# Optimization experiments

Measured on AMD Instinct MI355X. Metric: run time of the kernel, lower is better.

The kernel has to match this reference:

```python
import jax, jax.numpy as jnp
import numpy as np

N, D, E = 100000, 128, 600000  # nodes, feature dim, edges
EPS = 1e-5  # BatchNorm1d default eps


def setup_inputs() -> dict:
    key = jax.random.key(0)
    k = jax.random.split(key, 4)
    x = jax.random.normal(k[0], (N, D), jnp.float32)
    edge_index = jax.random.randint(k[1], (2, E), 0, N, jnp.int32)  # [src; dst]
    W = jax.random.normal(k[2], (D, D), jnp.float32) * (1.0 / np.sqrt(D))
    b = jnp.zeros((D,), jnp.float32)
    gamma = jnp.ones((D,), jnp.float32)
    beta = jnp.zeros((D,), jnp.float32)
    return dict(x=x, edge_index=edge_index, W=W, b=b, gamma=gamma, beta=beta)


def reference(x, edge_index, W, b, gamma, beta):
    # dropout p=0 -> identity
    src, dst = edge_index[0], edge_index[1]
    ones = jnp.ones((E,), x.dtype)
    deg_out = jnp.maximum(jax.ops.segment_sum(ones, src, num_segments=N), 1.0)
    deg_in = jnp.maximum(jax.ops.segment_sum(ones, dst, num_segments=N), 1.0)
    # GraphConv norm='both': D_out^{-1/2} on src side, sum-aggregate, D_in^{-1/2} on dst side
    h = x * jax.lax.rsqrt(deg_out)[:, None]            # [N, D]
    agg = jax.ops.segment_sum(h[src], dst, num_segments=N)  # gather+scatter over edges
    agg = agg * jax.lax.rsqrt(deg_in)[:, None]
    new_x = agg @ W + b                                 # linear after aggregation
    # residual (num_dst_nodes == N for a homogeneous graph)
    h = x + new_x
    # BatchNorm1d, training-mode batch statistics (biased variance)
    mean = jnp.mean(h, axis=0)
    var = jnp.var(h, axis=0)
    h = (h - mean) * jax.lax.rsqrt(var + EPS) * gamma + beta
    return jax.nn.relu(h)
```

## Files before the change

kernel.cpp:

```cpp
#include <hip/hip_runtime.h>
#include <math.h>

#define D 128
#define NGB 512
#define SLOTS 32
constexpr float EPS = 1e-5f;

typedef short v8s __attribute__((ext_vector_type(8)));
typedef float v4f __attribute__((ext_vector_type(4)));

__device__ __forceinline__ unsigned short f2bf(float f) {
    union { float f; unsigned u; } c; c.f = f;
    unsigned u = c.u;
    return (unsigned short)((u + 0x7FFFu + ((u >> 16) & 1u)) >> 16);
}
__device__ __forceinline__ float bf2f(unsigned short u) {
    union { unsigned u; float f; } c; c.u = ((unsigned)u) << 16; return c.f;
}

__global__ void fused_bucket_kernel(const int* __restrict__ src, const int* __restrict__ dst,
                                    int* __restrict__ deg_in, int* __restrict__ deg_out8,
                                    int* __restrict__ esrc, int n, int E) {
    int e = blockIdx.x * blockDim.x + threadIdx.x;
    if (e >= E) return;
    int s = src[e], d = dst[e];
    int pos = atomicAdd(&deg_in[d], 1);
    if (pos < SLOTS) esrc[((size_t)d << 5) | pos] = s;
    atomicAdd(&deg_out8[(size_t)(blockIdx.x & 7) * n + s], 1);
}

__global__ void rsdeg_kernel(const int* __restrict__ deg_out8, float* __restrict__ rs_out, int n) {
    int v = blockIdx.x * blockDim.x + threadIdx.x;
    if (v < n) {
        int s = 0;
        #pragma unroll
        for (int p = 0; p < 8; ++p) s += deg_out8[(size_t)p * n + v];
        rs_out[v] = rsqrtf(fmaxf((float)s, 1.0f));
    }
}

__global__ void xscale_kernel(const float4* __restrict__ x4, const float* __restrict__ rs_out,
                              ushort4* __restrict__ xb4, int total4) {
    int stride = gridDim.x * blockDim.x;
    for (int f = blockIdx.x * blockDim.x + threadIdx.x; f < total4; f += stride) {
        int row = f >> 5;
        float sc = rs_out[row];
        float4 v = x4[f];
        ushort4 o;
        o.x = f2bf(v.x * sc); o.y = f2bf(v.y * sc);
        o.z = f2bf(v.z * sc); o.w = f2bf(v.w * sc);
        xb4[f] = o;
    }
}

__global__ __launch_bounds__(256)
void agg_kernel(const ushort4* __restrict__ xb4, const int* __restrict__ deg_in,
                const int* __restrict__ esrc, ushort4* __restrict__ aggb4, int n) {
    int g = blockIdx.x * 8 + (threadIdx.x >> 5);
    int l32 = threadIdx.x & 31;
    if (g >= n) return;
    int deg = deg_in[g];
    int cnt = min(deg, SLOTS);
    const int* base = esrc + ((size_t)g << 5);
    float4 acc = make_float4(0.f, 0.f, 0.f, 0.f);
    int e = 0;
    for (; e + 3 < cnt; e += 4) {
        int s0 = base[e], s1 = base[e + 1], s2 = base[e + 2], s3 = base[e + 3];
        ushort4 u0 = xb4[(size_t)s0 * 32 + l32];
        ushort4 u1 = xb4[(size_t)s1 * 32 + l32];
        ushort4 u2 = xb4[(size_t)s2 * 32 + l32];
        ushort4 u3 = xb4[(size_t)s3 * 32 + l32];
        acc.x += bf2f(u0.x) + bf2f(u1.x) + bf2f(u2.x) + bf2f(u3.x);
        acc.y += bf2f(u0.y) + bf2f(u1.y) + bf2f(u2.y) + bf2f(u3.y);
        acc.z += bf2f(u0.z) + bf2f(u1.z) + bf2f(u2.z) + bf2f(u3.z);
        acc.w += bf2f(u0.w) + bf2f(u1.w) + bf2f(u2.w) + bf2f(u3.w);
    }
    for (; e < cnt; ++e) {
        int s0 = base[e];
        ushort4 u0 = xb4[(size_t)s0 * 32 + l32];
        acc.x += bf2f(u0.x);
        acc.y += bf2f(u0.y);
        acc.z += bf2f(u0.z);
        acc.w += bf2f(u0.w);
    }
    float si = rsqrtf(fmaxf((float)deg, 1.0f));
    ushort4 o;
    o.x = f2bf(acc.x * si);
    o.y = f2bf(acc.y * si);
    o.z = f2bf(acc.z * si);
    o.w = f2bf(acc.w * si);
    aggb4[(size_t)g * 32 + l32] = o;
}

__global__ void wconv_kernel(const float* __restrict__ W, ushort* __restrict__ wfrag) {
    int t = blockIdx.x * 256 + threadIdx.x;
    int lane = t & 63;
    int nt = (t >> 6) & 7;
    int kt = t >> 9;
    int n = nt * 16 + (lane & 15);
    int k0 = kt * 32 + (lane >> 4) * 8;
    ushort* dst = wfrag + (size_t)t * 8;
    #pragma unroll
    for (int j = 0; j < 8; ++j) dst[j] = f2bf(W[(size_t)(k0 + j) * D + n]);
}

__global__ __launch_bounds__(256, 2)
void gemm_mfma_kernel(const v8s* __restrict__ aggb8,
                      const v8s* __restrict__ wfrag8,
                      const float* __restrict__ b,
                      const float* __restrict__ x,
                      float* __restrict__ out,
                      float* __restrict__ bnpart, int n) {
    const int lane = threadIdx.x & 63;
    const int wave = threadIdx.x >> 6;
    const int gwave = blockIdx.x * 4 + wave;
    const int nwaves = gridDim.x * 4;
    const int ntiles = (n + 15) >> 4;
    const int c = lane & 15;
    const int s = lane >> 4;

    v8s wf[4][8];
    #pragma unroll
    for (int kt = 0; kt < 4; ++kt)
        #pragma unroll
        for (int nt = 0; nt < 8; ++nt)
            wf[kt][nt] = wfrag8[(kt * 8 + nt) * 64 + lane];

    float bv[8];
    #pragma unroll
    for (int nt = 0; nt < 8; ++nt) bv[nt] = b[nt * 16 + c];

    float hs[8], hq[8];
    #pragma unroll
    for (int nt = 0; nt < 8; ++nt) { hs[nt] = 0.f; hq[nt] = 0.f; }

    for (int tile = gwave; tile < ntiles; tile += nwaves) {
        const int row0 = tile * 16;
        int arow = row0 + c;
        if (arow >= n) arow = n - 1;

        v4f acc[8];
        #pragma unroll
        for (int nt = 0; nt < 8; ++nt) acc[nt] = (v4f)(0.f);

        #pragma unroll
        for (int kt = 0; kt < 4; ++kt) {
            v8s af = aggb8[(size_t)arow * 16 + kt * 4 + s];
            #pragma unroll
            for (int nt = 0; nt < 8; ++nt)
                acc[nt] = __builtin_amdgcn_mfma_f32_16x16x32_bf16(af, wf[kt][nt], acc[nt], 0, 0, 0);
        }

        #pragma unroll
        for (int j = 0; j < 4; ++j) {
            int m = row0 + s * 4 + j;
            if (m < n) {
                const float* xr = x + (size_t)m * D;
                float* orow = out + (size_t)m * D;
                #pragma unroll
                for (int nt = 0; nt < 8; ++nt) {
                    float h = acc[nt][j] + bv[nt] + xr[nt * 16 + c];
                    orow[nt * 16 + c] = h;
                    hs[nt] += h;
                    hq[nt] += h * h;
                }
            }
        }
    }

    #pragma unroll
    for (int nt = 0; nt < 8; ++nt) {
        hs[nt] += __shfl_xor(hs[nt], 16); hs[nt] += __shfl_xor(hs[nt], 32);
        hq[nt] += __shfl_xor(hq[nt], 16); hq[nt] += __shfl_xor(hq[nt], 32);
    }
    __shared__ float ls[4][128];
    __shared__ float lq[4][128];
    if (s == 0) {
        #pragma unroll
        for (int nt = 0; nt < 8; ++nt) {
            ls[wave][nt * 16 + c] = hs[nt];
            lq[wave][nt * 16 + c] = hq[nt];
        }
    }
    __syncthreads();
    const int t = threadIdx.x;
    if (t < 128) {
        float a = ls[0][t] + ls[1][t] + ls[2][t] + ls[3][t];
        bnpart[(size_t)t * NGB + blockIdx.x] = a;
    } else {
        int cc = t - 128;
        float a = lq[0][cc] + lq[1][cc] + lq[2][cc] + lq[3][cc];
        bnpart[(size_t)(128 + cc) * NGB + blockIdx.x] = a;
    }
}

__global__ __launch_bounds__(256)
void stats2_kernel(const float* __restrict__ partial, float* __restrict__ stats) {
    const int idx = blockIdx.x;
    const int t = threadIdx.x;
    float a = partial[(size_t)idx * NGB + t] + partial[(size_t)idx * NGB + 256 + t];
    #pragma unroll
    for (int off = 32; off >= 1; off >>= 1) a += __shfl_xor(a, off);
    __shared__ float w[4];
    if ((t & 63) == 0) w[t >> 6] = a;
    __syncthreads();
    if (t == 0) stats[idx] = w[0] + w[1] + w[2] + w[3];
}

__global__ void params_kernel(const float* __restrict__ stats, const float* __restrict__ gamma,
                              const float* __restrict__ beta, float* __restrict__ scale,
                              float* __restrict__ shift, float inv_n) {
    int c = threadIdx.x;
    if (c < D) {
        float mean = stats[c] * inv_n;
        float var = fmaxf(stats[D + c] * inv_n - mean * mean, 0.f);
        float inv = rsqrtf(var + EPS);
        float sc = gamma[c] * inv;
        scale[c] = sc;
        shift[c] = beta[c] - mean * sc;
    }
}

__global__ void final_kernel(float4* __restrict__ h4, const float4* __restrict__ scale4,
                             const float4* __restrict__ shift4, int total4) {
    int stride = gridDim.x * blockDim.x;
    for (int f = blockIdx.x * blockDim.x + threadIdx.x; f < total4; f += stride) {
        int c4 = f & 31;
        float4 v = h4[f];
        float4 s = scale4[c4];
        float4 sh = shift4[c4];
        float4 r;
        r.x = fmaxf(fmaf(v.x, s.x, sh.x), 0.f);
        r.y = fmaxf(fmaf(v.y, s.y, sh.y), 0.f);
        r.z = fmaxf(fmaf(v.z, s.z, sh.z), 0.f);
        r.w = fmaxf(fmaf(v.w, s.w, sh.w), 0.f);
        h4[f] = r;
    }
}

extern "C" void kernel_launch(void* const* d_in, const int* in_sizes, int n_in,
                              void* d_out, int out_size, void* d_ws, size_t ws_size,
                              hipStream_t stream) {
    const float* x     = (const float*)d_in[0];
    const int*   ei    = (const int*)d_in[1];
    const float* W     = (const float*)d_in[2];
    const float* b     = (const float*)d_in[3];
    const float* gamma = (const float*)d_in[4];
    const float* beta  = (const float*)d_in[5];

    const int E = in_sizes[1] / 2;
    const int n = in_sizes[0] / D;
    const int* src = ei;
    const int* dst = ei + E;

    unsigned short* xb    = (unsigned short*)d_ws;
    unsigned short* aggb  = xb + (size_t)n * D;
    unsigned short* wfrag = aggb + (size_t)n * D;
    int*   deg_in   = (int*)(wfrag + 2048 * 8);
    int*   deg_out8 = deg_in + n;
    float* rs_out   = (float*)(deg_out8 + 8 * (size_t)n);
    float* stats    = rs_out + n;
    float* scale    = stats + 256;
    float* shift    = scale + 128;
    float* bnpart   = shift + 128;

    int* esrc = (int*)d_out;

    hipMemsetAsync(deg_in, 0, 9 * (size_t)n * sizeof(int), stream);

    fused_bucket_kernel<<<(E + 255) / 256, 256, 0, stream>>>(src, dst, deg_in, deg_out8,
                                                             esrc, n, E);
    wconv_kernel<<<8, 256, 0, stream>>>(W, wfrag);
    rsdeg_kernel<<<(n + 255) / 256, 256, 0, stream>>>(deg_out8, rs_out, n);
    xscale_kernel<<<2048, 256, 0, stream>>>((const float4*)x, rs_out, (ushort4*)xb, n * 32);
    agg_kernel<<<(n + 7) / 8, 256, 0, stream>>>((const ushort4*)xb, deg_in, esrc,
                                                (ushort4*)aggb, n);
    gemm_mfma_kernel<<<NGB, 256, 0, stream>>>((const v8s*)aggb, (const v8s*)wfrag,
                                              b, x, (float*)d_out, bnpart, n);
    stats2_kernel<<<256, 256, 0, stream>>>(bnpart, stats);
    params_kernel<<<1, 128, 0, stream>>>(stats, gamma, beta, scale, shift, 1.0f / (float)n);
    final_kernel<<<4096, 256, 0, stream>>>((float4*)d_out, (const float4*)scale,
                                           (const float4*)shift, n * 32);
}
```

Before: 150.6 us.

## Fuse aggregation into MFMA GEMM via LDS and merge prep kernels

```diff
diff --git a/kernel.cpp b/kernel.cpp
--- a/kernel.cpp
+++ b/kernel.cpp
@@ -2,8 +2,9 @@
 #include <math.h>
 
 #define D 128
-#define NGB 512
 #define SLOTS 32
+#define WB 8
+#define XB 512
 constexpr float EPS = 1e-5f;
 
 typedef short v8s __attribute__((ext_vector_type(8)));
@@ -18,15 +19,39 @@
     union { unsigned u; float f; } c; c.u = ((unsigned)u) << 16; return c.f;
 }
 
-__global__ void fused_bucket_kernel(const int* __restrict__ src, const int* __restrict__ dst,
-                                    int* __restrict__ deg_in, int* __restrict__ deg_out8,
-                                    int* __restrict__ esrc, int n, int E) {
-    int e = blockIdx.x * blockDim.x + threadIdx.x;
-    if (e >= E) return;
-    int s = src[e], d = dst[e];
-    int pos = atomicAdd(&deg_in[d], 1);
-    if (pos < SLOTS) esrc[((size_t)d << 5) | pos] = s;
-    atomicAdd(&deg_out8[(size_t)(blockIdx.x & 7) * n + s], 1);
+__global__ void prep_kernel(const int* __restrict__ src, const int* __restrict__ dst,
+                            const float* __restrict__ W, const float4* __restrict__ x4,
+                            int* __restrict__ deg_in, int* __restrict__ deg_out8,
+                            int* __restrict__ esrc, unsigned short* __restrict__ wfrag,
+                            ushort4* __restrict__ xb4, int n, int E, int total4) {
+    const int bid = blockIdx.x;
+    const int tid = threadIdx.x;
+    if (bid < WB) {
+        int t = bid * 256 + tid;
+        int lane = t & 63;
+        int nt = (t >> 6) & 7;
+        int kt = t >> 9;
+        int col = nt * 16 + (lane & 15);
+        int k0 = kt * 32 + (lane >> 4) * 8;
+        unsigned short* dstp = wfrag + (size_t)t * 8;
+        #pragma unroll
+        for (int j = 0; j < 8; ++j) dstp[j] = f2bf(W[(size_t)(k0 + j) * D + col]);
+    } else if (bid < WB + XB) {
+        for (int f = (bid - WB) * 256 + tid; f < total4; f += XB * 256) {
+            float4 v = x4[f];
+            ushort4 o;
+            o.x = f2bf(v.x); o.y = f2bf(v.y); o.z = f2bf(v.z); o.w = f2bf(v.w);
+            xb4[f] = o;
+        }
+    } else {
+        int e = (bid - (WB + XB)) * 256 + tid;
+        if (e < E) {
+            int s = src[e], d = dst[e];
+            int pos = atomicAdd(&deg_in[d], 1);
+            if (pos < SLOTS) esrc[((size_t)d << 5) | pos] = s;
+            atomicAdd(&deg_out8[(size_t)(bid & 7) * n + s], 1);
+        }
+    }
 }
 
 __global__ void rsdeg_kernel(const int* __restrict__ deg_out8, float* __restrict__ rs_out, int n) {
@@ -39,85 +64,21 @@
     }
 }
 
-__global__ void xscale_kernel(const float4* __restrict__ x4, const float* __restrict__ rs_out,
-                              ushort4* __restrict__ xb4, int total4) {
-    int stride = gridDim.x * blockDim.x;
-    for (int f = blockIdx.x * blockDim.x + threadIdx.x; f < total4; f += stride) {
-        int row = f >> 5;
-        float sc = rs_out[row];
-        float4 v = x4[f];
-        ushort4 o;
-        o.x = f2bf(v.x * sc); o.y = f2bf(v.y * sc);
-        o.z = f2bf(v.z * sc); o.w = f2bf(v.w * sc);
-        xb4[f] = o;
-    }
-}
-
-__global__ __launch_bounds__(256)
-void agg_kernel(const ushort4* __restrict__ xb4, const int* __restrict__ deg_in,
-                const int* __restrict__ esrc, ushort4* __restrict__ aggb4, int n) {
-    int g = blockIdx.x * 8 + (threadIdx.x >> 5);
-    int l32 = threadIdx.x & 31;
-    if (g >= n) return;
-    int deg = deg_in[g];
-    int cnt = min(deg, SLOTS);
-    const int* base = esrc + ((size_t)g << 5);
-    float4 acc = make_float4(0.f, 0.f, 0.f, 0.f);
-    int e = 0;
-    for (; e + 3 < cnt; e += 4) {
-        int s0 = base[e], s1 = base[e + 1], s2 = base[e + 2], s3 = base[e + 3];
-        ushort4 u0 = xb4[(size_t)s0 * 32 + l32];
-        ushort4 u1 = xb4[(size_t)s1 * 32 + l32];
-        ushort4 u2 = xb4[(size_t)s2 * 32 + l32];
-        ushort4 u3 = xb4[(size_t)s3 * 32 + l32];
-        acc.x += bf2f(u0.x) + bf2f(u1.x) + bf2f(u2.x) + bf2f(u3.x);
-        acc.y += bf2f(u0.y) + bf2f(u1.y) + bf2f(u2.y) + bf2f(u3.y);
-        acc.z += bf2f(u0.z) + bf2f(u1.z) + bf2f(u2.z) + bf2f(u3.z);
-        acc.w += bf2f(u0.w) + bf2f(u1.w) + bf2f(u2.w) + bf2f(u3.w);
-    }
-    for (; e < cnt; ++e) {
-        int s0 = base[e];
-        ushort4 u0 = xb4[(size_t)s0 * 32 + l32];
-        acc.x += bf2f(u0.x);
-        acc.y += bf2f(u0.y);
-        acc.z += bf2f(u0.z);
-        acc.w += bf2f(u0.w);
-    }
-    float si = rsqrtf(fmaxf((float)deg, 1.0f));
-    ushort4 o;
-    o.x = f2bf(acc.x * si);
-    o.y = f2bf(acc.y * si);
-    o.z = f2bf(acc.z * si);
-    o.w = f2bf(acc.w * si);
-    aggb4[(size_t)g * 32 + l32] = o;
-}
-
-__global__ void wconv_kernel(const float* __restrict__ W, ushort* __restrict__ wfrag) {
-    int t = blockIdx.x * 256 + threadIdx.x;
-    int lane = t & 63;
-    int nt = (t >> 6) & 7;
-    int kt = t >> 9;
-    int n = nt * 16 + (lane & 15);
-    int k0 = kt * 32 + (lane >> 4) * 8;
-    ushort* dst = wfrag + (size_t)t * 8;
-    #pragma unroll
-    for (int j = 0; j < 8; ++j) dst[j] = f2bf(W[(size_t)(k0 + j) * D + n]);
-}
-
 __global__ __launch_bounds__(256, 2)
-void gemm_mfma_kernel(const v8s* __restrict__ aggb8,
-                      const v8s* __restrict__ wfrag8,
-                      const float* __restrict__ b,
-                      const float* __restrict__ x,
-                      float* __restrict__ out,
-                      float* __restrict__ bnpart, int n) {
-    const int lane = threadIdx.x & 63;
-    const int wave = threadIdx.x >> 6;
-    const int gwave = blockIdx.x * 4 + wave;
-    const int nwaves = gridDim.x * 4;
-    const int ntiles = (n + 15) >> 4;
+void agg_gemm_kernel(const ushort4* __restrict__ xb4, const float* __restrict__ rs_out,
+                     const int* __restrict__ deg_in, const int* __restrict__ esrc,
+                     const v8s* __restrict__ wfrag8, const float* __restrict__ b,
+                     const float* __restrict__ x, float* __restrict__ out,
+                     float* __restrict__ bnpart, int n) {
+    __shared__ unsigned short lds_a[64][128];
+    __shared__ float ls[4][128];
+    __shared__ float lq[4][128];
+    const int tid = threadIdx.x;
+    const int row0 = blockIdx.x * 64;
+    const int lane = tid & 63;
+    const int wave = tid >> 6;
     const int c = lane & 15;
-    const int s = lane >> 4;
+    const int s16 = lane >> 4;
 
     v8s wf[4][8];
     #pragma unroll
@@ -126,44 +87,72 @@
         for (int nt = 0; nt < 8; ++nt)
             wf[kt][nt] = wfrag8[(kt * 8 + nt) * 64 + lane];
 
+    const int g32 = tid >> 5;
+    const int l32 = tid & 31;
+    for (int r8 = 0; r8 < 8; ++r8) {
+        int lr = r8 * 8 + g32;
+        int row = row0 + lr;
+        if (row < n) {
+            int deg = deg_in[row];
+            int cnt = min(deg, SLOTS);
+            int sE = (l32 < cnt) ? esrc[((size_t)row << 5) + l32] : 0;
+            float rv = (l32 < cnt) ? rs_out[sE] : 0.f;
+            float4 acc = make_float4(0.f, 0.f, 0.f, 0.f);
+            for (int e = 0; e < cnt; ++e) {
+                int s = __shfl(sE, e, 32);
+                float sc = __shfl(rv, e, 32);
+                ushort4 u = xb4[(size_t)s * 32 + l32];
+                acc.x += bf2f(u.x) * sc;
+                acc.y += bf2f(u.y) * sc;
+                acc.z += bf2f(u.z) * sc;
+                acc.w += bf2f(u.w) * sc;
+            }
+            float si = rsqrtf(fmaxf((float)deg, 1.0f));
+            ushort4 o;
+            o.x = f2bf(acc.x * si); o.y = f2bf(acc.y * si);
+            o.z = f2bf(acc.z * si); o.w = f2bf(acc.w * si);
+            int jsw = l32 ^ ((lr & 7) << 2);
+            *(ushort4*)&lds_a[lr][jsw * 4] = o;
+        }
+    }
+    __syncthreads();
+
+    const int lr0 = wave * 16;
+
     float bv[8];
     #pragma unroll
     for (int nt = 0; nt < 8; ++nt) bv[nt] = b[nt * 16 + c];
 
+    v4f acc[8];
+    #pragma unroll
+    for (int nt = 0; nt < 8; ++nt) acc[nt] = (v4f)(0.f);
+
+    #pragma unroll
+    for (int kt = 0; kt < 4; ++kt) {
+        int lr = lr0 + c;
+        int jj = ((kt * 4 + s16) * 2) ^ ((lr & 7) << 2);
+        v8s af = *(const v8s*)&lds_a[lr][jj * 4];
+        #pragma unroll
+        for (int nt = 0; nt < 8; ++nt)
+            acc[nt] = __builtin_amdgcn_mfma_f32_16x16x32_bf16(af, wf[kt][nt], acc[nt], 0, 0, 0);
+    }
+
     float hs[8], hq[8];
     #pragma unroll
     for (int nt = 0; nt < 8; ++nt) { hs[nt] = 0.f; hq[nt] = 0.f; }
 
-    for (int tile = gwave; tile < ntiles; tile += nwaves) {
-        const int row0 = tile * 16;
-        int arow = row0 + c;
-        if (arow >= n) arow = n - 1;
-
-        v4f acc[8];
-        #pragma unroll
-        for (int nt = 0; nt < 8; ++nt) acc[nt] = (v4f)(0.f);
-
-        #pragma unroll
-        for (int kt = 0; kt < 4; ++kt) {
-            v8s af = aggb8[(size_t)arow * 16 + kt * 4 + s];
+    #pragma unroll
+    for (int j = 0; j < 4; ++j) {
+        int m = row0 + lr0 + s16 * 4 + j;
+        if (m < n) {
+            const float* xr = x + (size_t)m * D;
+            float* orow = out + (size_t)m * D;
             #pragma unroll
-            for (int nt = 0; nt < 8; ++nt)
-                acc[nt] = __builtin_amdgcn_mfma_f32_16x16x32_bf16(af, wf[kt][nt], acc[nt], 0, 0, 0);
-        }
-
-        #pragma unroll
-        for (int j = 0; j < 4; ++j) {
-            int m = row0 + s * 4 + j;
-            if (m < n) {
-                const float* xr = x + (size_t)m * D;
-                float* orow = out + (size_t)m * D;
-                #pragma unroll
-                for (int nt = 0; nt < 8; ++nt) {
-                    float h = acc[nt][j] + bv[nt] + xr[nt * 16 + c];
-                    orow[nt * 16 + c] = h;
-                    hs[nt] += h;
-                    hq[nt] += h * h;
-                }
+            for (int nt = 0; nt < 8; ++nt) {
+                float h = acc[nt][j] + bv[nt] + xr[nt * 16 + c];
+                orow[nt * 16 + c] = h;
+                hs[nt] += h;
+                hq[nt] += h * h;
             }
         }
     }
@@ -173,9 +162,7 @@
         hs[nt] += __shfl_xor(hs[nt], 16); hs[nt] += __shfl_xor(hs[nt], 32);
         hq[nt] += __shfl_xor(hq[nt], 16); hq[nt] += __shfl_xor(hq[nt], 32);
     }
-    __shared__ float ls[4][128];
-    __shared__ float lq[4][128];
-    if (s == 0) {
+    if (s16 == 0) {
         #pragma unroll
         for (int nt = 0; nt < 8; ++nt) {
             ls[wave][nt * 16 + c] = hs[nt];
@@ -183,22 +170,22 @@
         }
     }
     __syncthreads();
-    const int t = threadIdx.x;
-    if (t < 128) {
-        float a = ls[0][t] + ls[1][t] + ls[2][t] + ls[3][t];
-        bnpart[(size_t)t * NGB + blockIdx.x] = a;
+    if (tid < 128) {
+        float a = ls[0][tid] + ls[1][tid] + ls[2][tid] + ls[3][tid];
+        bnpart[(size_t)tid * gridDim.x + blockIdx.x] = a;
     } else {
-        int cc = t - 128;
+        int cc = tid - 128;
         float a = lq[0][cc] + lq[1][cc] + lq[2][cc] + lq[3][cc];
-        bnpart[(size_t)(128 + cc) * NGB + blockIdx.x] = a;
+        bnpart[(size_t)(128 + cc) * gridDim.x + blockIdx.x] = a;
     }
 }
 
 __global__ __launch_bounds__(256)
-void stats2_kernel(const float* __restrict__ partial, float* __restrict__ stats) {
+void stats2_kernel(const float* __restrict__ partial, float* __restrict__ stats, int NT) {
     const int idx = blockIdx.x;
     const int t = threadIdx.x;
-    float a = partial[(size_t)idx * NGB + t] + partial[(size_t)idx * NGB + 256 + t];
+    float a = 0.f;
+    for (int k = t; k < NT; k += 256) a += partial[(size_t)idx * NT + k];
     #pragma unroll
     for (int off = 32; off >= 1; off >>= 1) a += __shfl_xor(a, off);
     __shared__ float w[4];
@@ -253,31 +240,30 @@
     const int* src = ei;
     const int* dst = ei + E;
 
+    const int NT = (n + 63) / 64;
+
     unsigned short* xb    = (unsigned short*)d_ws;
-    unsigned short* aggb  = xb + (size_t)n * D;
-    unsigned short* wfrag = aggb + (size_t)n * D;
+    unsigned short* wfrag = xb + (size_t)n * D;
     int*   deg_in   = (int*)(wfrag + 2048 * 8);
     int*   deg_out8 = deg_in + n;
-    float* rs_out   = (float*)(deg_out8 + 8 * (size_t)n);
+    int*   esrc     = deg_out8 + 8 * (size_t)n;
+    float* rs_out   = (float*)(esrc + (size_t)n * SLOTS);
     float* stats    = rs_out + n;
     float* scale    = stats + 256;
     float* shift    = scale + 128;
     float* bnpart   = shift + 128;
 
-    int* esrc = (int*)d_out;
-
     hipMemsetAsync(deg_in, 0, 9 * (size_t)n * sizeof(int), stream);
 
-    fused_bucket_kernel<<<(E + 255) / 256, 256, 0, stream>>>(src, dst, deg_in, deg_out8,
-                                                             esrc, n, E);
-    wconv_kernel<<<8, 256, 0, stream>>>(W, wfrag);
+    const int GB = (E + 255) / 256;
+    prep_kernel<<<WB + XB + GB, 256, 0, stream>>>(src, dst, W, (const float4*)x,
+                                                  deg_in, deg_out8, esrc, wfrag,
+                                                  (ushort4*)xb, n, E, n * 32);
     rsdeg_kernel<<<(n + 255) / 256, 256, 0, stream>>>(deg_out8, rs_out, n);
-    xscale_kernel<<<2048, 256, 0, stream>>>((const float4*)x, rs_out, (ushort4*)xb, n * 32);
-    agg_kernel<<<(n + 7) / 8, 256, 0, stream>>>((const ushort4*)xb, deg_in, esrc,
-                                                (ushort4*)aggb, n);
-    gemm_mfma_kernel<<<NGB, 256, 0, stream>>>((const v8s*)aggb, (const v8s*)wfrag,
-                                              b, x, (float*)d_out, bnpart, n);
-    stats2_kernel<<<256, 256, 0, stream>>>(bnpart, stats);
+    agg_gemm_kernel<<<NT, 256, 0, stream>>>((const ushort4*)xb, rs_out, deg_in, esrc,
+                                            (const v8s*)wfrag, b, x, (float*)d_out,
+                                            bnpart, n);
+    stats2_kernel<<<256, 256, 0, stream>>>(bnpart, stats, NT);
     params_kernel<<<1, 128, 0, stream>>>(stats, gamma, beta, scale, shift, 1.0f / (float)n);
     final_kernel<<<4096, 256, 0, stream>>>((float4*)d_out, (const float4*)scale,
                                            (const float4*)shift, n * 32);
```

New measurement: 193.7 us. +28.6%, slower.

## Merge bucketing, W conversion and x bf16 cast; apply out-degree scale in aggregation

Applied to the files above, without the earlier changes.

```diff
diff --git a/kernel.cpp b/kernel.cpp
--- a/kernel.cpp
+++ b/kernel.cpp
@@ -4,6 +4,8 @@
 #define D 128
 #define NGB 512
 #define SLOTS 32
+#define WB 8
+#define XB 512
 constexpr float EPS = 1e-5f;
 
 typedef short v8s __attribute__((ext_vector_type(8)));
@@ -18,15 +20,39 @@
     union { unsigned u; float f; } c; c.u = ((unsigned)u) << 16; return c.f;
 }
 
-__global__ void fused_bucket_kernel(const int* __restrict__ src, const int* __restrict__ dst,
-                                    int* __restrict__ deg_in, int* __restrict__ deg_out8,
-                                    int* __restrict__ esrc, int n, int E) {
-    int e = blockIdx.x * blockDim.x + threadIdx.x;
-    if (e >= E) return;
-    int s = src[e], d = dst[e];
-    int pos = atomicAdd(&deg_in[d], 1);
-    if (pos < SLOTS) esrc[((size_t)d << 5) | pos] = s;
-    atomicAdd(&deg_out8[(size_t)(blockIdx.x & 7) * n + s], 1);
+__global__ void prep_kernel(const int* __restrict__ src, const int* __restrict__ dst,
+                            const float* __restrict__ W, const float4* __restrict__ x4,
+                            int* __restrict__ deg_in, int* __restrict__ deg_out8,
+                            int* __restrict__ esrc, unsigned short* __restrict__ wfrag,
+                            ushort4* __restrict__ xb4, int n, int E, int total4) {
+    const int bid = blockIdx.x;
+    const int tid = threadIdx.x;
+    if (bid < WB) {
+        int t = bid * 256 + tid;
+        int lane = t & 63;
+        int nt = (t >> 6) & 7;
+        int kt = t >> 9;
+        int col = nt * 16 + (lane & 15);
+        int k0 = kt * 32 + (lane >> 4) * 8;
+        unsigned short* dstp = wfrag + (size_t)t * 8;
+        #pragma unroll
+        for (int j = 0; j < 8; ++j) dstp[j] = f2bf(W[(size_t)(k0 + j) * D + col]);
+    } else if (bid < WB + XB) {
+        for (int f = (bid - WB) * 256 + tid; f < total4; f += XB * 256) {
+            float4 v = x4[f];
+            ushort4 o;
+            o.x = f2bf(v.x); o.y = f2bf(v.y); o.z = f2bf(v.z); o.w = f2bf(v.w);
+            xb4[f] = o;
+        }
+    } else {
+        int e = (bid - (WB + XB)) * 256 + tid;
+        if (e < E) {
+            int s = src[e], d = dst[e];
+            int pos = atomicAdd(&deg_in[d], 1);
+            if (pos < SLOTS) esrc[((size_t)d << 5) | pos] = s;
+            atomicAdd(&deg_out8[(size_t)(bid & 7) * n + s], 1);
+        }
+    }
 }
 
 __global__ void rsdeg_kernel(const int* __restrict__ deg_out8, float* __restrict__ rs_out, int n) {
@@ -39,49 +65,41 @@
     }
 }
 
-__global__ void xscale_kernel(const float4* __restrict__ x4, const float* __restrict__ rs_out,
-                              ushort4* __restrict__ xb4, int total4) {
-    int stride = gridDim.x * blockDim.x;
-    for (int f = blockIdx.x * blockDim.x + threadIdx.x; f < total4; f += stride) {
-        int row = f >> 5;
-        float sc = rs_out[row];
-        float4 v = x4[f];
-        ushort4 o;
-        o.x = f2bf(v.x * sc); o.y = f2bf(v.y * sc);
-        o.z = f2bf(v.z * sc); o.w = f2bf(v.w * sc);
-        xb4[f] = o;
-    }
-}
-
 __global__ __launch_bounds__(256)
-void agg_kernel(const ushort4* __restrict__ xb4, const int* __restrict__ deg_in,
-                const int* __restrict__ esrc, ushort4* __restrict__ aggb4, int n) {
+void agg_kernel(const ushort4* __restrict__ xb4, const float* __restrict__ rs_out,
+                const int* __restrict__ deg_in, const int* __restrict__ esrc,
+                ushort4* __restrict__ aggb4, int n) {
     int g = blockIdx.x * 8 + (threadIdx.x >> 5);
     int l32 = threadIdx.x & 31;
     if (g >= n) return;
     int deg = deg_in[g];
     int cnt = min(deg, SLOTS);
-    const int* base = esrc + ((size_t)g << 5);
+    int sE = (l32 < cnt) ? esrc[((size_t)g << 5) + l32] : 0;
+    float rv = (l32 < cnt) ? rs_out[sE] : 0.f;
     float4 acc = make_float4(0.f, 0.f, 0.f, 0.f);
     int e = 0;
     for (; e + 3 < cnt; e += 4) {
-        int s0 = base[e], s1 = base[e + 1], s2 = base[e + 2], s3 = base[e + 3];
+        int s0 = __shfl(sE, e, 32),     s1 = __shfl(sE, e + 1, 32);
+        int s2 = __shfl(sE, e + 2, 32), s3 = __shfl(sE, e + 3, 32);
+        float c0 = __shfl(rv, e, 32),     c1 = __shfl(rv, e + 1, 32);
+        float c2 = __shfl(rv, e + 2, 32), c3 = __shfl(rv, e + 3, 32);
         ushort4 u0 = xb4[(size_t)s0 * 32 + l32];
         ushort4 u1 = xb4[(size_t)s1 * 32 + l32];
         ushort4 u2 = xb4[(size_t)s2 * 32 + l32];
         ushort4 u3 = xb4[(size_t)s3 * 32 + l32];
-        acc.x += bf2f(u0.x) + bf2f(u1.x) + bf2f(u2.x) + bf2f(u3.x);
-        acc.y += bf2f(u0.y) + bf2f(u1.y) + bf2f(u2.y) + bf2f(u3.y);
-        acc.z += bf2f(u0.z) + bf2f(u1.z) + bf2f(u2.z) + bf2f(u3.z);
-        acc.w += bf2f(u0.w) + bf2f(u1.w) + bf2f(u2.w) + bf2f(u3.w);
+        acc.x += bf2f(u0.x) * c0 + bf2f(u1.x) * c1 + bf2f(u2.x) * c2 + bf2f(u3.x) * c3;
+        acc.y += bf2f(u0.y) * c0 + bf2f(u1.y) * c1 + bf2f(u2.y) * c2 + bf2f(u3.y) * c3;
+        acc.z += bf2f(u0.z) * c0 + bf2f(u1.z) * c1 + bf2f(u2.z) * c2 + bf2f(u3.z) * c3;
+        acc.w += bf2f(u0.w) * c0 + bf2f(u1.w) * c1 + bf2f(u2.w) * c2 + bf2f(u3.w) * c3;
     }
     for (; e < cnt; ++e) {
-        int s0 = base[e];
+        int s0 = __shfl(sE, e, 32);
+        float c0 = __shfl(rv, e, 32);
         ushort4 u0 = xb4[(size_t)s0 * 32 + l32];
-        acc.x += bf2f(u0.x);
-        acc.y += bf2f(u0.y);
-        acc.z += bf2f(u0.z);
-        acc.w += bf2f(u0.w);
+        acc.x += bf2f(u0.x) * c0;
+        acc.y += bf2f(u0.y) * c0;
+        acc.z += bf2f(u0.z) * c0;
+        acc.w += bf2f(u0.w) * c0;
     }
     float si = rsqrtf(fmaxf((float)deg, 1.0f));
     ushort4 o;
@@ -90,18 +108,6 @@
     o.z = f2bf(acc.z * si);
     o.w = f2bf(acc.w * si);
     aggb4[(size_t)g * 32 + l32] = o;
-}
-
-__global__ void wconv_kernel(const float* __restrict__ W, ushort* __restrict__ wfrag) {
-    int t = blockIdx.x * 256 + threadIdx.x;
-    int lane = t & 63;
-    int nt = (t >> 6) & 7;
-    int kt = t >> 9;
-    int n = nt * 16 + (lane & 15);
-    int k0 = kt * 32 + (lane >> 4) * 8;
-    ushort* dst = wfrag + (size_t)t * 8;
-    #pragma unroll
-    for (int j = 0; j < 8; ++j) dst[j] = f2bf(W[(size_t)(k0 + j) * D + n]);
 }
 
 __global__ __launch_bounds__(256, 2)
@@ -268,12 +274,12 @@
 
     hipMemsetAsync(deg_in, 0, 9 * (size_t)n * sizeof(int), stream);
 
-    fused_bucket_kernel<<<(E + 255) / 256, 256, 0, stream>>>(src, dst, deg_in, deg_out8,
-                                                             esrc, n, E);
-    wconv_kernel<<<8, 256, 0, stream>>>(W, wfrag);
+    const int GB = (E + 255) / 256;
+    prep_kernel<<<WB + XB + GB, 256, 0, stream>>>(src, dst, W, (const float4*)x,
+                                                  deg_in, deg_out8, esrc, wfrag,
+                                                  (ushort4*)xb, n, E, n * 32);
     rsdeg_kernel<<<(n + 255) / 256, 256, 0, stream>>>(deg_out8, rs_out, n);
-    xscale_kernel<<<2048, 256, 0, stream>>>((const float4*)x, rs_out, (ushort4*)xb, n * 32);
-    agg_kernel<<<(n + 7) / 8, 256, 0, stream>>>((const ushort4*)xb, deg_in, esrc,
+    agg_kernel<<<(n + 7) / 8, 256, 0, stream>>>((const ushort4*)xb, rs_out, deg_in, esrc,
                                                 (ushort4*)aggb, n);
     gemm_mfma_kernel<<<NGB, 256, 0, stream>>>((const v8s*)aggb, (const v8s*)wfrag,
                                               b, x, (float*)d_out, bnpart, n);
```

Result: faster. 144.5 us (-4.0%).
